# Kernel tuning notes

Hardware: AMD Instinct MI355X
Metric: run time of the kernel (lower is better)

Reference implementation:

```python
import jax, jax.numpy as jnp
import numpy as np

B, L, HSIZE = 16, 512, 1024
H, D = 16, 64  # HHEAD = HSIZE/base, HBASE = 64

def setup_inputs() -> dict:
    key = jax.random.key(0)
    ks = jax.random.split(key, 10)
    inp = {
        'v': jax.random.normal(ks[0], (B, L, HSIZE), jnp.float32),
        'k': jax.random.normal(ks[1], (B, L, HSIZE), jnp.float32),
        'q': jax.random.normal(ks[2], (B, L, HSIZE), jnp.float32),
        'img_abs': jax.random.normal(ks[3], (B, L, HSIZE), jnp.float32),
        'Wv': jax.random.normal(ks[4], (HSIZE, HSIZE), jnp.float32) * 0.02,
        'Wk': jax.random.normal(ks[5], (HSIZE, HSIZE), jnp.float32) * 0.02,
        'Wq': jax.random.normal(ks[6], (HSIZE, HSIZE), jnp.float32) * 0.02,
        'Wm': jax.random.normal(ks[7], (HSIZE, HSIZE), jnp.float32) * 0.02,
        'abs_mask': jax.random.bernoulli(ks[8], 0.1, (B, 1, L, L)),
        'mask': jax.random.bernoulli(ks[9], 0.1, (B, 1, L, L)),
    }
    return inp

def reference(v, k, q, img_abs, Wv, Wk, Wq, Wm, abs_mask, mask):
    nb = q.shape[0]
    # Linear (no bias) then split heads: [B, L, HSIZE] -> [B, H, L, D]
    def heads(x):
        return x.reshape(nb, -1, H, D).transpose(0, 2, 1, 3)
    vh = heads(v @ Wv.T)
    kh = heads(k @ Wk.T)
    qh = heads(q @ Wq.T)
    ph = heads(img_abs)
    scale = 1.0 / jnp.sqrt(jnp.asarray(D, qh.dtype))
    # modulate: attention of q over positional features, residual-added to q
    s1 = jnp.einsum('bhqd,bhpd->bhqp', qh, ph) * scale
    s1 = jnp.where(abs_mask, jnp.asarray(-1e9, s1.dtype), s1)
    qh = qh + jnp.einsum('bhqp,bhpd->bhqd', jax.nn.softmax(s1, axis=-1), ph)
    # main attention (dropout = identity in eval mode)
    s2 = jnp.einsum('bhqd,bhkd->bhqk', qh, kh) * scale
    s2 = jnp.where(mask, jnp.asarray(-1e9, s2.dtype), s2)
    atted = jnp.einsum('bhqk,bhkd->bhqd', jax.nn.softmax(s2, axis=-1), vh)
    atted = atted.transpose(0, 2, 1, 3).reshape(nb, -1, H * D)
    return atted @ Wm.T
```

## Files before the change

### kernel.cpp

```cpp
#include <hip/hip_runtime.h>

typedef unsigned short u16;
typedef unsigned int u32;
typedef unsigned long long u64;
typedef __attribute__((ext_vector_type(8))) short short8;
typedef __attribute__((ext_vector_type(4))) float f32x4;

#define NB 16
#define SL 512
#define HS 1024
#define NHEAD 16
#define HD 64
#define NTOKC (16L * 512 * 1024)
#define NWC   (1024L * 1024)

typedef const __attribute__((address_space(1))) u32* gas_t;
typedef __attribute__((address_space(3))) u32* las_t;

__device__ __forceinline__ void gld16(const u16* g, u16* l) {
  __builtin_amdgcn_global_load_lds((gas_t)g, (las_t)l, 16, 0, 0);
}

__device__ __forceinline__ u16 f2bf(float f) {
  union { float f; unsigned u; } c; c.f = f;
  unsigned r = c.u + 0x7FFFu + ((c.u >> 16) & 1u);
  return (u16)(r >> 16);
}
__device__ __forceinline__ float bf2f(u16 u) {
  union { float f; unsigned u; } c; c.u = ((unsigned)u) << 16;
  return c.f;
}

__global__ __launch_bounds__(256) void cvt4(const float* __restrict__ v,
                                            const float* __restrict__ k,
                                            const float* __restrict__ q,
                                            const float* __restrict__ img,
                                            u16* __restrict__ ovk,
                                            u16* __restrict__ xq,
                                            u16* __restrict__ pb, long n) {
  int which = blockIdx.y;
  const float* in = which == 0 ? v : which == 1 ? k : which == 2 ? q : img;
  u16* out = which == 0 ? ovk : which == 1 ? ovk + n : which == 2 ? xq : pb;
  long i = ((long)blockIdx.x * 256 + threadIdx.x) * 4;
  if (i >= n) return;
  float4 f = *(const float4*)(in + i);
  uint2 u;
  u.x = (unsigned)f2bf(f.x) | ((unsigned)f2bf(f.y) << 16);
  u.y = (unsigned)f2bf(f.z) | ((unsigned)f2bf(f.w) << 16);
  *(uint2*)(out + i) = u;
}

__global__ __launch_bounds__(256) void cvt_w4(const float* __restrict__ a,
                                              const float* __restrict__ b,
                                              const float* __restrict__ c,
                                              const float* __restrict__ d,
                                              u16* __restrict__ o, long n) {
  const float* in = (blockIdx.y == 0) ? a : (blockIdx.y == 1) ? b
                     : (blockIdx.y == 2) ? c : d;
  u16* out = o + (long)blockIdx.y * n;
  long i = ((long)blockIdx.x * 256 + threadIdx.x) * 4;
  if (i >= n) return;
  float4 f = *(const float4*)(in + i);
  uint2 u;
  u.x = (unsigned)f2bf(f.x) | ((unsigned)f2bf(f.y) << 16);
  u.y = (unsigned)f2bf(f.z) | ((unsigned)f2bf(f.w) << 16);
  *(uint2*)(out + i) = u;
}

__global__ __launch_bounds__(256) void pack_mask(const int* __restrict__ m0,
                                                 const int* __restrict__ m1,
                                                 u64* __restrict__ o0,
                                                 u64* __restrict__ o1, long n) {
  long i = (long)blockIdx.x * 256 + threadIdx.x;
  const int* m = blockIdx.y ? m1 : m0;
  u64* o = blockIdx.y ? o1 : o0;
  u64 bits = __ballot(m[i] != 0);
  if ((threadIdx.x & 63) == 0) o[i >> 6] = bits;
}

__global__ __launch_bounds__(256) void gemm_p3(const u16* __restrict__ Avk,
                                               const u16* __restrict__ Aq,
                                               const u16* __restrict__ W4,
                                               u16* __restrict__ Cb) {
  __shared__ u16 As[128 * 64];
  __shared__ u16 Bs[128 * 64];
  const int tid = threadIdx.x;
  const int wave = tid >> 6, lane = tid & 63;
  const int quad = lane >> 4, l16 = lane & 15;
  const int l7 = l16 & 7;
  const int sel = blockIdx.x >> 6;
  const int row0 = (blockIdx.x & 63) * 128, col0 = blockIdx.y * 128;
  const int wm = (wave >> 1) * 64, wn = (wave & 1) * 64;
  const int lrow = lane >> 3;
  const int scb = (lane & 7) ^ lrow;
  const int K = HS, N = HS;

  const u16* A = (sel == 2) ? Aq : Avk + (long)sel * NTOKC;
  const u16* W = W4 + (long)sel * NWC;
  u16* C = Cb + (long)sel * NTOKC;

  f32x4 acc[4][4];
#pragma unroll
  for (int mt = 0; mt < 4; ++mt)
#pragma unroll
    for (int nt = 0; nt < 4; ++nt) acc[mt][nt] = (f32x4){0.f, 0.f, 0.f, 0.f};

  const u16* Ab = A + (long)row0 * K;
  const u16* Wb = W + (long)col0 * K;

  for (int k0 = 0; k0 < K; k0 += 64) {
    __syncthreads();
#pragma unroll
    for (int it = 0; it < 4; ++it) {
      int seg = wave * 4 + it;
      int r = seg * 8 + lrow;
      gld16(Ab + (long)r * K + k0 + scb * 8, As + seg * 512);
      gld16(Wb + (long)r * K + k0 + scb * 8, Bs + seg * 512);
    }
    __syncthreads();
#pragma unroll
    for (int kt = 0; kt < 2; ++kt) {
      short8 af[4], bw[4];
#pragma unroll
      for (int mt = 0; mt < 4; ++mt)
        af[mt] = *(const short8*)(As + (wm + mt * 16 + l16) * 64 +
                                  (((kt * 4 + quad) ^ l7) * 8));
#pragma unroll
      for (int nt = 0; nt < 4; ++nt)
        bw[nt] = *(const short8*)(Bs + (wn + nt * 16 + l16) * 64 +
                                  (((kt * 4 + quad) ^ l7) * 8));
#pragma unroll
      for (int mt = 0; mt < 4; ++mt)
#pragma unroll
        for (int nt = 0; nt < 4; ++nt)
          acc[mt][nt] = __builtin_amdgcn_mfma_f32_16x16x32_bf16(
              af[mt], bw[nt], acc[mt][nt], 0, 0, 0);
    }
  }
#pragma unroll
  for (int mt = 0; mt < 4; ++mt)
#pragma unroll
    for (int nt = 0; nt < 4; ++nt)
#pragma unroll
      for (int i = 0; i < 4; ++i) {
        long r = row0 + wm + mt * 16 + quad * 4 + i;
        long c = col0 + wn + nt * 16 + l16;
        C[r * N + c] = f2bf(acc[mt][nt][i]);
      }
}

__global__ __launch_bounds__(256, 4) void gemm_f(const u16* __restrict__ A,
                                                 const u16* __restrict__ W,
                                                 float* __restrict__ C) {
  __shared__ u16 As[64 * 64];
  __shared__ u16 Bs[128 * 64];
  const int tid = threadIdx.x;
  const int wave = tid >> 6, lane = tid & 63;
  const int quad = lane >> 4, l16 = lane & 15;
  const int l7 = l16 & 7;
  const int row0 = blockIdx.x * 64, col0 = blockIdx.y * 128;
  const int wm = (wave >> 1) * 32, wn = (wave & 1) * 64;
  const int lrow = lane >> 3;
  const int scb = (lane & 7) ^ lrow;
  const int K = HS, N = HS;

  f32x4 acc[2][4];
#pragma unroll
  for (int mt = 0; mt < 2; ++mt)
#pragma unroll
    for (int nt = 0; nt < 4; ++nt) acc[mt][nt] = (f32x4){0.f, 0.f, 0.f, 0.f};

  const u16* Ab = A + (long)row0 * K;
  const u16* Wb = W + (long)col0 * K;

  for (int k0 = 0; k0 < K; k0 += 64) {
    __syncthreads();
#pragma unroll
    for (int it = 0; it < 2; ++it) {
      int seg = wave * 2 + it;
      gld16(Ab + (long)(seg * 8 + lrow) * K + k0 + scb * 8, As + seg * 512);
    }
#pragma unroll
    for (int it = 0; it < 4; ++it) {
      int seg = wave * 4 + it;
      gld16(Wb + (long)(seg * 8 + lrow) * K + k0 + scb * 8, Bs + seg * 512);
    }
    __syncthreads();
#pragma unroll
    for (int kt = 0; kt < 2; ++kt) {
      short8 af[2], bw[4];
#pragma unroll
      for (int mt = 0; mt < 2; ++mt)
        af[mt] = *(const short8*)(As + (wm + mt * 16 + l16) * 64 +
                                  (((kt * 4 + quad) ^ l7) * 8));
#pragma unroll
      for (int nt = 0; nt < 4; ++nt)
        bw[nt] = *(const short8*)(Bs + (wn + nt * 16 + l16) * 64 +
                                  (((kt * 4 + quad) ^ l7) * 8));
#pragma unroll
      for (int mt = 0; mt < 2; ++mt)
#pragma unroll
        for (int nt = 0; nt < 4; ++nt)
          acc[mt][nt] = __builtin_amdgcn_mfma_f32_16x16x32_bf16(
              af[mt], bw[nt], acc[mt][nt], 0, 0, 0);
    }
  }
#pragma unroll
  for (int mt = 0; mt < 2; ++mt)
#pragma unroll
    for (int nt = 0; nt < 4; ++nt)
#pragma unroll
      for (int i = 0; i < 4; ++i) {
        long r = row0 + wm + mt * 16 + quad * 4 + i;
        long c = col0 + wn + nt * 16 + l16;
        C[r * N + c] = acc[mt][nt][i];
      }
}

__global__ __launch_bounds__(256) void attn(const u16* __restrict__ Qp,
                                            const u16* __restrict__ Kp,
                                            const u16* __restrict__ Vp,
                                            const u32* __restrict__ Bits,
                                            u16* __restrict__ Op,
                                            int residual) {
  __shared__ u16 Ks[64][72];
  __shared__ u16 Vs[64][72];
  __shared__ u16 Ps[64][72];
  const int tid = threadIdx.x;
  const int wave = tid >> 6, lane = tid & 63;
  const int quad = lane >> 4, l16 = lane & 15;
  const int qt = blockIdx.x, h = blockIdx.y, b = blockIdx.z;
  const int q0 = qt * 64;
  const long bs = (long)SL * HS;
  const u16* Qb = Qp + (long)b * bs + h * HD;
  const u16* Kb = Kp + (long)b * bs + h * HD;
  const u16* Vb = Vp + (long)b * bs + h * HD;
  const u32* Mb = Bits + (long)b * SL * 16;

  short8 qf[2];
#pragma unroll
  for (int kt = 0; kt < 2; ++kt) {
    int row = q0 + wave * 16 + l16;
    qf[kt] = *(const short8*)(Qb + (long)row * HS + kt * 32 + quad * 8);
  }

  float l_i[4] = {0.f, 0.f, 0.f, 0.f};
  f32x4 o[4];
#pragma unroll
  for (int nt = 0; nt < 4; ++nt) o[nt] = (f32x4){0.f, 0.f, 0.f, 0.f};

  const int sr = tid >> 2, sds = (tid & 3) * 16;
  const int vcol = sr ^ (((sds >> 4) & 3) << 4);

  for (int t = 0; t < 8; ++t) {
    const int k0 = t * 64;
    __syncthreads();
    {
      const uint4* sk = (const uint4*)(Kb + (long)(k0 + sr) * HS + sds);
      *(uint4*)&Ks[sr][sds] = sk[0];
      *(uint4*)&Ks[sr][sds + 8] = sk[1];
      uint4 v0 = *(const uint4*)(Vb + (long)(k0 + sr) * HS + sds);
      uint4 v1 = *(const uint4*)(Vb + (long)(k0 + sr) * HS + sds + 8);
      union { uint4 q[2]; u16 e[16]; } tv;
      tv.q[0] = v0; tv.q[1] = v1;
#pragma unroll
      for (int j = 0; j < 16; ++j) Vs[sds + j][vcol] = tv.e[j];
    }
    __syncthreads();
    f32x4 s[4];
#pragma unroll
    for (int nt = 0; nt < 4; ++nt) s[nt] = (f32x4){0.f, 0.f, 0.f, 0.f};
#pragma unroll
    for (int kt = 0; kt < 2; ++kt)
#pragma unroll
      for (int nt = 0; nt < 4; ++nt) {
        short8 bk = *(const short8*)&Ks[nt * 16 + l16][kt * 32 + quad * 8];
        s[nt] = __builtin_amdgcn_mfma_f32_16x16x32_bf16(qf[kt], bk, s[nt], 0, 0, 0);
      }
#pragma unroll
    for (int i = 0; i < 4; ++i) {
      int gr = q0 + wave * 16 + quad * 4 + i;
      uint2 mw = *(const uint2*)&Mb[(long)gr * 16 + t * 2];
#pragma unroll
      for (int nt = 0; nt < 4; ++nt) {
        u32 w = (nt & 2) ? mw.y : mw.x;
        int msk = (w >> ((nt & 1) * 16 + l16)) & 1;
        float p = msk ? 0.f : __expf(s[nt][i] * 0.125f);
        l_i[i] += p;
        Ps[wave * 16 + quad * 4 + i][nt * 16 + l16] = f2bf(p);
      }
    }
    __syncthreads();
#pragma unroll
    for (int kt = 0; kt < 2; ++kt) {
      short8 ap = *(const short8*)&Ps[wave * 16 + l16][kt * 32 + quad * 8];
#pragma unroll
      for (int nt = 0; nt < 4; ++nt) {
        short8 bv = *(const short8*)&Vs[nt * 16 + l16]
                                      [(kt * 32 + quad * 8) ^ ((nt & 3) << 4)];
        o[nt] = __builtin_amdgcn_mfma_f32_16x16x32_bf16(ap, bv, o[nt], 0, 0, 0);
      }
    }
  }
  u16* Ob = Op + (long)b * bs + h * HD;
#pragma unroll
  for (int i = 0; i < 4; ++i) {
    float rs = l_i[i];
#pragma unroll
    for (int off = 8; off >= 1; off >>= 1) rs += __shfl_xor(rs, off, 64);
    float inv = 1.f / rs;
    int r = q0 + wave * 16 + quad * 4 + i;
#pragma unroll
    for (int nt = 0; nt < 4; ++nt) {
      float val = o[nt][i] * inv;
      if (residual) val += bf2f(Qb[(long)r * HS + nt * 16 + l16]);
      Ob[(long)r * HS + nt * 16 + l16] = f2bf(val);
    }
  }
}

extern "C" void kernel_launch(void* const* d_in, const int* in_sizes, int n_in,
                              void* d_out, int out_size, void* d_ws,
                              size_t ws_size, hipStream_t stream) {
  const float* v   = (const float*)d_in[0];
  const float* k   = (const float*)d_in[1];
  const float* q   = (const float*)d_in[2];
  const float* img = (const float*)d_in[3];
  const float* Wv  = (const float*)d_in[4];
  const float* Wk  = (const float*)d_in[5];
  const float* Wq  = (const float*)d_in[6];
  const float* Wm  = (const float*)d_in[7];
  const int* absm  = (const int*)d_in[8];
  const int* mask  = (const int*)d_in[9];
  float* out = (float*)d_out;

  const long NTOK = NTOKC;
  const long NW   = NWC;
  const long NM   = (long)NB * SL * SL;
  u16* ovk = (u16*)d_out;
  u16* ws  = (u16*)d_ws;
  u16* xq  = ws;
  u16* pb  = ws + 1 * NTOK;
  u16* vh  = ws + 2 * NTOK;
  u16* kh  = ws + 3 * NTOK;
  u16* qh  = ws + 4 * NTOK;
  u16* w4  = ws + 5 * NTOK;
  u64* bt0 = (u64*)(w4 + 4 * NW);
  u64* bt1 = bt0 + NM / 64;
  u16* qm  = xq;
  u16* att = qh;

  cvt4<<<dim3((unsigned)(NTOK / 1024), 4), 256, 0, stream>>>(v, k, q, img,
                                                             ovk, xq, pb, NTOK);
  cvt_w4<<<dim3((unsigned)(NW / 1024), 4), 256, 0, stream>>>(Wv, Wk, Wq, Wm, w4, NW);
  pack_mask<<<dim3((unsigned)(NM / 256), 2), 256, 0, stream>>>(absm, mask, bt0, bt1, NM);

  gemm_p3<<<dim3(192, 8), 256, 0, stream>>>(ovk, xq, w4, vh);

  dim3 ga(SL / 64, NHEAD, NB);
  attn<<<ga, 256, 0, stream>>>(qh, pb, pb, (const u32*)bt0, qm, 1);
  attn<<<ga, 256, 0, stream>>>(qm, kh, vh, (const u32*)bt1, att, 0);

  gemm_f<<<dim3(NB * SL / 64, HS / 128), 256, 0, stream>>>(att, w4 + 3 * NW, out);
}
```

Baseline: 425.5 us.

## Fuse both attention stages into one kernel, prefetch K/V, merge prep kernels

Merges the three preprocessing kernels (activation cast, weight cast, mask bit-packing) into one launch with a 2D grid partitioned by blockIdx.y. Fuses the positional-modulation attention and the main attention into a single kernel. The modulated query is formed in registers via LDS instead of being written to and re-read from global memory. Each K/V tile is prefetched into registers one iteration ahead, and one of the three __syncthreads per tile is dropped. The risks are higher register pressure and an extra bf16 rounding when adding the residual to the query.

```diff
diff --git a/kernel.cpp b/kernel.cpp
--- a/kernel.cpp
+++ b/kernel.cpp
@@ -13,6 +13,7 @@
 #define HD 64
 #define NTOKC (16L * 512 * 1024)
 #define NWC   (1024L * 1024)
+#define NMC   (16L * 512 * 512)
 
 typedef const __attribute__((address_space(1))) u32* gas_t;
 typedef __attribute__((address_space(3))) u32* las_t;
@@ -31,51 +32,46 @@
   return c.f;
 }
 
-__global__ __launch_bounds__(256) void cvt4(const float* __restrict__ v,
-                                            const float* __restrict__ k,
-                                            const float* __restrict__ q,
-                                            const float* __restrict__ img,
-                                            u16* __restrict__ ovk,
-                                            u16* __restrict__ xq,
-                                            u16* __restrict__ pb, long n) {
-  int which = blockIdx.y;
-  const float* in = which == 0 ? v : which == 1 ? k : which == 2 ? q : img;
-  u16* out = which == 0 ? ovk : which == 1 ? ovk + n : which == 2 ? xq : pb;
-  long i = ((long)blockIdx.x * 256 + threadIdx.x) * 4;
-  if (i >= n) return;
-  float4 f = *(const float4*)(in + i);
-  uint2 u;
-  u.x = (unsigned)f2bf(f.x) | ((unsigned)f2bf(f.y) << 16);
-  u.y = (unsigned)f2bf(f.z) | ((unsigned)f2bf(f.w) << 16);
-  *(uint2*)(out + i) = u;
-}
-
-__global__ __launch_bounds__(256) void cvt_w4(const float* __restrict__ a,
-                                              const float* __restrict__ b,
-                                              const float* __restrict__ c,
-                                              const float* __restrict__ d,
-                                              u16* __restrict__ o, long n) {
-  const float* in = (blockIdx.y == 0) ? a : (blockIdx.y == 1) ? b
-                     : (blockIdx.y == 2) ? c : d;
-  u16* out = o + (long)blockIdx.y * n;
-  long i = ((long)blockIdx.x * 256 + threadIdx.x) * 4;
-  if (i >= n) return;
-  float4 f = *(const float4*)(in + i);
-  uint2 u;
-  u.x = (unsigned)f2bf(f.x) | ((unsigned)f2bf(f.y) << 16);
-  u.y = (unsigned)f2bf(f.z) | ((unsigned)f2bf(f.w) << 16);
-  *(uint2*)(out + i) = u;
-}
-
-__global__ __launch_bounds__(256) void pack_mask(const int* __restrict__ m0,
-                                                 const int* __restrict__ m1,
-                                                 u64* __restrict__ o0,
-                                                 u64* __restrict__ o1, long n) {
-  long i = (long)blockIdx.x * 256 + threadIdx.x;
-  const int* m = blockIdx.y ? m1 : m0;
-  u64* o = blockIdx.y ? o1 : o0;
-  u64 bits = __ballot(m[i] != 0);
-  if ((threadIdx.x & 63) == 0) o[i >> 6] = bits;
+__global__ __launch_bounds__(256) void prep(
+    const float* __restrict__ v, const float* __restrict__ k,
+    const float* __restrict__ q, const float* __restrict__ img,
+    const float* __restrict__ Wv, const float* __restrict__ Wk,
+    const float* __restrict__ Wq, const float* __restrict__ Wm,
+    const int* __restrict__ absm, const int* __restrict__ mask,
+    u16* __restrict__ ovk, u16* __restrict__ xq, u16* __restrict__ pb,
+    u16* __restrict__ w4, u64* __restrict__ bits) {
+  const int y = blockIdx.y;
+  const long bx = blockIdx.x;
+  if (y < 4) {
+    const float* in = y == 0 ? v : y == 1 ? k : y == 2 ? q : img;
+    u16* out = y == 0 ? ovk : y == 1 ? ovk + NTOKC : y == 2 ? xq : pb;
+    long i = (bx * 256 + threadIdx.x) * 4;
+    float4 f = *(const float4*)(in + i);
+    uint2 u;
+    u.x = (unsigned)f2bf(f.x) | ((unsigned)f2bf(f.y) << 16);
+    u.y = (unsigned)f2bf(f.z) | ((unsigned)f2bf(f.w) << 16);
+    *(uint2*)(out + i) = u;
+  } else if (y == 4) {
+    if (bx >= 4096) return;
+    long i = bx * 1024 + threadIdx.x * 4;
+    int j = (int)(i >> 20);
+    const float* in = j == 0 ? Wv : j == 1 ? Wk : j == 2 ? Wq : Wm;
+    long off = i & (NWC - 1);
+    float4 f = *(const float4*)(in + off);
+    uint2 u;
+    u.x = (unsigned)f2bf(f.x) | ((unsigned)f2bf(f.y) << 16);
+    u.y = (unsigned)f2bf(f.z) | ((unsigned)f2bf(f.w) << 16);
+    *(uint2*)(w4 + i) = u;
+  } else {
+#pragma unroll
+    for (int rep = 0; rep < 4; ++rep) {
+      long i = (bx * 4 + rep) * 256 + threadIdx.x;
+      const int* m = (i >= NMC) ? mask : absm;
+      long off = i & (NMC - 1);
+      u64 bset = __ballot(m[off] != 0);
+      if ((threadIdx.x & 63) == 0) bits[i >> 6] = bset;
+    }
+  }
 }
 
 __global__ __launch_bounds__(256) void gemm_p3(const u16* __restrict__ Avk,
@@ -217,12 +213,75 @@
       }
 }
 
-__global__ __launch_bounds__(256) void attn(const u16* __restrict__ Qp,
-                                            const u16* __restrict__ Kp,
-                                            const u16* __restrict__ Vp,
-                                            const u32* __restrict__ Bits,
-                                            u16* __restrict__ Op,
-                                            int residual) {
+__device__ __forceinline__ void attn_stage(
+    const u16* __restrict__ Kb, const u16* __restrict__ Vb,
+    const u32* __restrict__ Mb, int q0, short8 qf[2], float l_i[4],
+    f32x4 o[4], u16 (*Ks)[72], u16 (*Vs)[72], u16 (*Ps)[72],
+    int wave, int quad, int l16, int sr, int sds, int vcol) {
+  uint4 kp0 = *(const uint4*)(Kb + (long)sr * HS + sds);
+  uint4 kp1 = *(const uint4*)(Kb + (long)sr * HS + sds + 8);
+  uint4 vp0 = *(const uint4*)(Vb + (long)sr * HS + sds);
+  uint4 vp1 = *(const uint4*)(Vb + (long)sr * HS + sds + 8);
+  for (int t = 0; t < 8; ++t) {
+    __syncthreads();
+    *(uint4*)&Ks[sr][sds] = kp0;
+    *(uint4*)&Ks[sr][sds + 8] = kp1;
+    {
+      union { uint4 q[2]; u16 e[16]; } tv;
+      tv.q[0] = vp0; tv.q[1] = vp1;
+#pragma unroll
+      for (int j = 0; j < 16; ++j) Vs[sds + j][vcol] = tv.e[j];
+    }
+    __syncthreads();
+    if (t < 7) {
+      const u16* Kn = Kb + (long)((t + 1) * 64 + sr) * HS;
+      kp0 = *(const uint4*)(Kn + sds);
+      kp1 = *(const uint4*)(Kn + sds + 8);
+      const u16* Vn = Vb + (long)((t + 1) * 64 + sr) * HS;
+      vp0 = *(const uint4*)(Vn + sds);
+      vp1 = *(const uint4*)(Vn + sds + 8);
+    }
+    f32x4 s[4];
+#pragma unroll
+    for (int nt = 0; nt < 4; ++nt) s[nt] = (f32x4){0.f, 0.f, 0.f, 0.f};
+#pragma unroll
+    for (int kt = 0; kt < 2; ++kt)
+#pragma unroll
+      for (int nt = 0; nt < 4; ++nt) {
+        short8 bk = *(const short8*)&Ks[nt * 16 + l16][kt * 32 + quad * 8];
+        s[nt] = __builtin_amdgcn_mfma_f32_16x16x32_bf16(qf[kt], bk, s[nt], 0, 0, 0);
+      }
+#pragma unroll
+    for (int i = 0; i < 4; ++i) {
+      int gr = q0 + wave * 16 + quad * 4 + i;
+      uint2 mw = *(const uint2*)&Mb[(long)gr * 16 + t * 2];
+#pragma unroll
+      for (int nt = 0; nt < 4; ++nt) {
+        u32 w = (nt & 2) ? mw.y : mw.x;
+        int msk = (w >> ((nt & 1) * 16 + l16)) & 1;
+        float p = msk ? 0.f : __expf(s[nt][i] * 0.125f);
+        l_i[i] += p;
+        Ps[wave * 16 + quad * 4 + i][nt * 16 + l16] = f2bf(p);
+      }
+    }
+#pragma unroll
+    for (int kt = 0; kt < 2; ++kt) {
+      short8 ap = *(const short8*)&Ps[wave * 16 + l16][kt * 32 + quad * 8];
+#pragma unroll
+      for (int nt = 0; nt < 4; ++nt) {
+        short8 bv = *(const short8*)&Vs[nt * 16 + l16]
+                                      [(kt * 32 + quad * 8) ^ ((nt & 3) << 4)];
+        o[nt] = __builtin_amdgcn_mfma_f32_16x16x32_bf16(ap, bv, o[nt], 0, 0, 0);
+      }
+    }
+  }
+}
+
+__global__ __launch_bounds__(256) void attn_fused(
+    const u16* __restrict__ Qp, const u16* __restrict__ Pbp,
+    const u16* __restrict__ Kp, const u16* __restrict__ Vp,
+    const u32* __restrict__ B0, const u32* __restrict__ B1,
+    u16* __restrict__ Op) {
   __shared__ u16 Ks[64][72];
   __shared__ u16 Vs[64][72];
   __shared__ u16 Ps[64][72];
@@ -233,75 +292,50 @@
   const int q0 = qt * 64;
   const long bs = (long)SL * HS;
   const u16* Qb = Qp + (long)b * bs + h * HD;
+  const u16* Pb = Pbp + (long)b * bs + h * HD;
   const u16* Kb = Kp + (long)b * bs + h * HD;
   const u16* Vb = Vp + (long)b * bs + h * HD;
-  const u32* Mb = Bits + (long)b * SL * 16;
+  const u32* M0 = B0 + (long)b * SL * 16;
+  const u32* M1 = B1 + (long)b * SL * 16;
+  const int sr = tid >> 2, sds = (tid & 3) * 16;
+  const int vcol = sr ^ (((sds >> 4) & 3) << 4);
 
   short8 qf[2];
 #pragma unroll
-  for (int kt = 0; kt < 2; ++kt) {
-    int row = q0 + wave * 16 + l16;
-    qf[kt] = *(const short8*)(Qb + (long)row * HS + kt * 32 + quad * 8);
-  }
+  for (int kt = 0; kt < 2; ++kt)
+    qf[kt] = *(const short8*)(Qb + (long)(q0 + wave * 16 + l16) * HS +
+                              kt * 32 + quad * 8);
 
   float l_i[4] = {0.f, 0.f, 0.f, 0.f};
   f32x4 o[4];
 #pragma unroll
   for (int nt = 0; nt < 4; ++nt) o[nt] = (f32x4){0.f, 0.f, 0.f, 0.f};
 
-  const int sr = tid >> 2, sds = (tid & 3) * 16;
-  const int vcol = sr ^ (((sds >> 4) & 3) << 4);
-
-  for (int t = 0; t < 8; ++t) {
-    const int k0 = t * 64;
-    __syncthreads();
-    {
-      const uint4* sk = (const uint4*)(Kb + (long)(k0 + sr) * HS + sds);
-      *(uint4*)&Ks[sr][sds] = sk[0];
-      *(uint4*)&Ks[sr][sds + 8] = sk[1];
-      uint4 v0 = *(const uint4*)(Vb + (long)(k0 + sr) * HS + sds);
-      uint4 v1 = *(const uint4*)(Vb + (long)(k0 + sr) * HS + sds + 8);
-      union { uint4 q[2]; u16 e[16]; } tv;
-      tv.q[0] = v0; tv.q[1] = v1;
-#pragma unroll
-      for (int j = 0; j < 16; ++j) Vs[sds + j][vcol] = tv.e[j];
-    }
-    __syncthreads();
-    f32x4 s[4];
-#pragma unroll
-    for (int nt = 0; nt < 4; ++nt) s[nt] = (f32x4){0.f, 0.f, 0.f, 0.f};
-#pragma unroll
-    for (int kt = 0; kt < 2; ++kt)
-#pragma unroll
-      for (int nt = 0; nt < 4; ++nt) {
-        short8 bk = *(const short8*)&Ks[nt * 16 + l16][kt * 32 + quad * 8];
-        s[nt] = __builtin_amdgcn_mfma_f32_16x16x32_bf16(qf[kt], bk, s[nt], 0, 0, 0);
-      }
-#pragma unroll
-    for (int i = 0; i < 4; ++i) {
-      int gr = q0 + wave * 16 + quad * 4 + i;
-      uint2 mw = *(const uint2*)&Mb[(long)gr * 16 + t * 2];
-#pragma unroll
-      for (int nt = 0; nt < 4; ++nt) {
-        u32 w = (nt & 2) ? mw.y : mw.x;
-        int msk = (w >> ((nt & 1) * 16 + l16)) & 1;
-        float p = msk ? 0.f : __expf(s[nt][i] * 0.125f);
-        l_i[i] += p;
-        Ps[wave * 16 + quad * 4 + i][nt * 16 + l16] = f2bf(p);
-      }
-    }
-    __syncthreads();
-#pragma unroll
-    for (int kt = 0; kt < 2; ++kt) {
-      short8 ap = *(const short8*)&Ps[wave * 16 + l16][kt * 32 + quad * 8];
-#pragma unroll
-      for (int nt = 0; nt < 4; ++nt) {
-        short8 bv = *(const short8*)&Vs[nt * 16 + l16]
-                                      [(kt * 32 + quad * 8) ^ ((nt & 3) << 4)];
-        o[nt] = __builtin_amdgcn_mfma_f32_16x16x32_bf16(ap, bv, o[nt], 0, 0, 0);
-      }
-    }
-  }
+  attn_stage(Pb, Pb, M0, q0, qf, l_i, o, Ks, Vs, Ps, wave, quad, l16, sr, sds, vcol);
+
+#pragma unroll
+  for (int i = 0; i < 4; ++i) {
+    float rs = l_i[i];
+#pragma unroll
+    for (int off = 8; off >= 1; off >>= 1) rs += __shfl_xor(rs, off, 64);
+    float inv = 1.f / rs;
+#pragma unroll
+    for (int nt = 0; nt < 4; ++nt)
+      Ps[wave * 16 + quad * 4 + i][nt * 16 + l16] = f2bf(o[nt][i] * inv);
+    l_i[i] = 0.f;
+  }
+#pragma unroll
+  for (int kt = 0; kt < 2; ++kt) {
+    short8 t8 = *(const short8*)&Ps[wave * 16 + l16][kt * 32 + quad * 8];
+#pragma unroll
+    for (int j = 0; j < 8; ++j)
+      qf[kt][j] = (short)f2bf(bf2f((u16)t8[j]) + bf2f((u16)qf[kt][j]));
+  }
+#pragma unroll
+  for (int nt = 0; nt < 4; ++nt) o[nt] = (f32x4){0.f, 0.f, 0.f, 0.f};
+
+  attn_stage(Kb, Vb, M1, q0, qf, l_i, o, Ks, Vs, Ps, wave, quad, l16, sr, sds, vcol);
+
   u16* Ob = Op + (long)b * bs + h * HD;
 #pragma unroll
   for (int i = 0; i < 4; ++i) {
@@ -311,11 +345,8 @@
     float inv = 1.f / rs;
     int r = q0 + wave * 16 + quad * 4 + i;
 #pragma unroll
-    for (int nt = 0; nt < 4; ++nt) {
-      float val = o[nt][i] * inv;
-      if (residual) val += bf2f(Qb[(long)r * HS + nt * 16 + l16]);
-      Ob[(long)r * HS + nt * 16 + l16] = f2bf(val);
-    }
+    for (int nt = 0; nt < 4; ++nt)
+      Ob[(long)r * HS + nt * 16 + l16] = f2bf(o[nt][i] * inv);
   }
 }
 
@@ -336,7 +367,7 @@
 
   const long NTOK = NTOKC;
   const long NW   = NWC;
-  const long NM   = (long)NB * SL * SL;
+  const long NM   = NMC;
   u16* ovk = (u16*)d_out;
   u16* ws  = (u16*)d_ws;
   u16* xq  = ws;
@@ -347,19 +378,12 @@
   u16* w4  = ws + 5 * NTOK;
   u64* bt0 = (u64*)(w4 + 4 * NW);
   u64* bt1 = bt0 + NM / 64;
-  u16* qm  = xq;
-  u16* att = qh;
-
-  cvt4<<<dim3((unsigned)(NTOK / 1024), 4), 256, 0, stream>>>(v, k, q, img,
-                                                             ovk, xq, pb, NTOK);
-  cvt_w4<<<dim3((unsigned)(NW / 1024), 4), 256, 0, stream>>>(Wv, Wk, Wq, Wm, w4, NW);
-  pack_mask<<<dim3((unsigned)(NM / 256), 2), 256, 0, stream>>>(absm, mask, bt0, bt1, NM);
-
+  u16* att = xq;
+
+  prep<<<dim3(8192, 6), 256, 0, stream>>>(v, k, q, img, Wv, Wk, Wq, Wm,
+                                          absm, mask, ovk, xq, pb, w4, bt0);
   gemm_p3<<<dim3(192, 8), 256, 0, stream>>>(ovk, xq, w4, vh);
-
-  dim3 ga(SL / 64, NHEAD, NB);
-  attn<<<ga, 256, 0, stream>>>(qh, pb, pb, (const u32*)bt0, qm, 1);
-  attn<<<ga, 256, 0, stream>>>(qm, kh, vh, (const u32*)bt1, att, 0);
-
+  attn_fused<<<dim3(SL / 64, NHEAD, NB), 256, 0, stream>>>(
+      qh, pb, kh, vh, (const u32*)bt0, (const u32*)bt1, att);
   gemm_f<<<dim3(NB * SL / 64, HS / 128), 256, 0, stream>>>(att, w4 + 3 * NW, out);
 }
```

Result: faster. 385.0 us (-9.5%).
